# Kernel tuning notes

Measured on AMD Instinct MI355X. Metric: run time of the kernel, lower is better.

Reference implementation:

```python
import jax, jax.numpy as jnp
import numpy as np

EPS = 1e-6
NEG_SLOPE_VEC = 0.2   # VNLeakyReLU default in Pocket2Mol
NEG_SLOPE_SCA = 0.01  # torch nn.LeakyReLU default


def _gvlinear(sca, vec, Wv1, Wv2, Ws, Wg, bg):
    # vec: (n, c_in, 3); Wv1: (c_in, h); Wv2: (h, c_out)
    vh = jnp.einsum('nci,ch->nhi', vec, Wv1)            # VNLinear 1 (no bias)
    vnorm = jnp.sqrt(jnp.sum(vh * vh, axis=-1))          # (n, h)
    out_sca = jnp.concatenate([vnorm, sca], axis=-1) @ Ws  # (n, s_out), no bias
    out_vec = jnp.einsum('nhi,ho->noi', vh, Wv2)         # VNLinear 2 (no bias)
    gate = jax.nn.sigmoid(out_sca @ Wg + bg)[..., None]  # (n, c_out, 1)
    return out_sca, gate * out_vec


def _vn_leaky_relu(vec, Wd):
    # vec: (n, c, 3); Wd: (c, c) learned direction map (no bias)
    d = jnp.einsum('nci,co->noi', vec, Wd)
    dot = jnp.sum(vec * d, axis=-1, keepdims=True)
    d_sq = jnp.sum(d * d, axis=-1, keepdims=True)
    proj = vec - (dot / (d_sq + EPS)) * d
    return NEG_SLOPE_VEC * vec + (1.0 - NEG_SLOPE_VEC) * jnp.where(dot >= 0, vec, proj)


def setup_inputs() -> dict:
    key = jax.random.key(0)
    ks = jax.random.split(key, 13)
    N, M = 400000, 200000
    in_sca, in_vec = 256, 64
    hs, hv = 128, 32
    dh1 = max(in_vec, hv)  # GVLinear layer1 hidden = 64
    dh2 = max(hv, 1)       # GVLinear layer2 hidden = 32

    def w(k, shape, fan_in):
        return jax.random.normal(k, shape, jnp.float32) / np.float32(np.sqrt(fan_in))

    return {
        'h_att_scalar': jax.random.normal(ks[0], (N, in_sca), jnp.float32),
        'h_att_vector': jax.random.normal(ks[1], (N, in_vec, 3), jnp.float32),
        'idx_ligans': jax.random.randint(ks[2], (M,), 0, N),
        # ---- layer 1: GVPerceptronVN (GVLinear + activations) ----
        'Wv1_1': w(ks[3], (in_vec, dh1), in_vec),
        'Wv2_1': w(ks[4], (dh1, hv), dh1),
        'Ws_1':  w(ks[5], (dh1 + in_sca, hs), dh1 + in_sca),
        'Wg_1':  w(ks[6], (hs, hv), hs),
        'bg_1':  jnp.zeros((hv,), jnp.float32),
        'Wd_1':  w(ks[7], (hv, hv), hv),
        # ---- layer 2: GVLinear to (1, 1) ----
        'Wv1_2': w(ks[8], (hv, dh2), hv),
        'Wv2_2': w(ks[9], (dh2, 1), dh2),
        'Ws_2':  w(ks[10], (dh2 + hs, 1), dh2 + hs),
        'Wg_2':  w(ks[11], (1, 1), 1),
        'bg_2':  jnp.zeros((1,), jnp.float32),
    }


def reference(h_att_scalar, h_att_vector, idx_ligans,
              Wv1_1, Wv2_1, Ws_1, Wg_1, bg_1, Wd_1,
              Wv1_2, Wv2_2, Ws_2, Wg_2, bg_2):
    # gather ligand rows
    sca = h_att_scalar[idx_ligans]
    vec = h_att_vector[idx_ligans]
    # GVPerceptronVN
    sca, vec = _gvlinear(sca, vec, Wv1_1, Wv2_1, Ws_1, Wg_1, bg_1)
    vec = _vn_leaky_relu(vec, Wd_1)
    sca = jnp.where(sca >= 0, sca, NEG_SLOPE_SCA * sca)
    # GVLinear -> (1, 1); only scalar branch is returned
    out_sca, _ = _gvlinear(sca, vec, Wv1_2, Wv2_2, Ws_2, Wg_2, bg_2)
    return out_sca  # (M, 1)
```

## Files before the change

### kernel.cpp

```cpp
#include <hip/hip_runtime.h>
#include <math.h>


#define NSV 0.2f
#define NSS 0.01f

__global__ __launch_bounds__(256) void k1_kernel(
    const float* __restrict__ hvec,
    const int*   __restrict__ idx,
    const float* __restrict__ Wv1,
    const float* __restrict__ Wv2,
    float* __restrict__ vnorm_ws,
    float* __restrict__ ovec_ws,
    int M)
{
    __shared__ __align__(16) float sWv1[64*64];
    __shared__ __align__(16) float sWv2[64*32];
    __shared__ __align__(16) float sv[32*196];
    __shared__ int sidx[32];

    const int tid  = threadIdx.x;
    const int row0 = blockIdx.x * 32;

    #pragma unroll
    for (int p = 0; p < 4; ++p) {
        int lin = p*256 + tid;
        *(float4*)&sWv1[lin*4] = *(const float4*)&Wv1[lin*4];
    }
    #pragma unroll
    for (int p = 0; p < 2; ++p) {
        int lin = p*256 + tid;
        *(float4*)&sWv2[lin*4] = *(const float4*)&Wv2[lin*4];
    }
    if (tid < 32) {
        int m = row0 + tid;
        sidx[tid] = idx[m < M ? m : M-1];
    }
    __syncthreads();

    #pragma unroll
    for (int p = 0; p < 6; ++p) {
        int lin = p*256 + tid;
        int r = lin / 48, e4 = lin % 48;
        *(float4*)&sv[r*196 + e4*4] = *(const float4*)&hvec[(size_t)sidx[r]*192 + e4*4];
    }
    __syncthreads();

    const int tx = tid & 15;
    const int ty = tid >> 4;
    float acc[2][4][3];
    #pragma unroll
    for (int a = 0; a < 2; ++a)
        #pragma unroll
        for (int b = 0; b < 4; ++b)
            #pragma unroll
            for (int c = 0; c < 3; ++c) acc[a][b][c] = 0.f;

    for (int c = 0; c < 64; ++c) {
        float av[2][3];
        #pragma unroll
        for (int rr = 0; rr < 2; ++rr) {
            int base = (ty*2 + rr)*196 + c*3;
            av[rr][0] = sv[base+0]; av[rr][1] = sv[base+1]; av[rr][2] = sv[base+2];
        }
        float4 w4 = *(const float4*)&sWv1[c*64 + tx*4];
        float wv[4] = {w4.x, w4.y, w4.z, w4.w};
        #pragma unroll
        for (int rr = 0; rr < 2; ++rr)
            #pragma unroll
            for (int hh = 0; hh < 4; ++hh)
                #pragma unroll
                for (int x = 0; x < 3; ++x)
                    acc[rr][hh][x] += av[rr][x] * wv[hh];
    }

    #pragma unroll
    for (int rr = 0; rr < 2; ++rr) {
        int m = row0 + ty*2 + rr;
        float4 vn;
        vn.x = sqrtf(acc[rr][0][0]*acc[rr][0][0] + acc[rr][0][1]*acc[rr][0][1] + acc[rr][0][2]*acc[rr][0][2]);
        vn.y = sqrtf(acc[rr][1][0]*acc[rr][1][0] + acc[rr][1][1]*acc[rr][1][1] + acc[rr][1][2]*acc[rr][1][2]);
        vn.z = sqrtf(acc[rr][2][0]*acc[rr][2][0] + acc[rr][2][1]*acc[rr][2][1] + acc[rr][2][2]*acc[rr][2][2]);
        vn.w = sqrtf(acc[rr][3][0]*acc[rr][3][0] + acc[rr][3][1]*acc[rr][3][1] + acc[rr][3][2]*acc[rr][3][2]);
        if (m < M) *(float4*)&vnorm_ws[(size_t)m*64 + tx*4] = vn;
    }

    __syncthreads();
    #pragma unroll
    for (int rr = 0; rr < 2; ++rr)
        #pragma unroll
        for (int hh = 0; hh < 4; ++hh)
            #pragma unroll
            for (int x = 0; x < 3; ++x)
                sv[(ty*2 + rr)*196 + (tx*4 + hh)*3 + x] = acc[rr][hh][x];
    __syncthreads();

    const int to = tid & 7;
    const int r2 = tid >> 3;
    float oa[4][3];
    #pragma unroll
    for (int a = 0; a < 4; ++a)
        #pragma unroll
        for (int c = 0; c < 3; ++c) oa[a][c] = 0.f;

    for (int h = 0; h < 64; ++h) {
        int base = r2*196 + h*3;
        float a0 = sv[base+0], a1 = sv[base+1], a2 = sv[base+2];
        float4 w4 = *(const float4*)&sWv2[h*32 + to*4];
        float wv[4] = {w4.x, w4.y, w4.z, w4.w};
        #pragma unroll
        for (int oo = 0; oo < 4; ++oo) {
            oa[oo][0] += a0*wv[oo];
            oa[oo][1] += a1*wv[oo];
            oa[oo][2] += a2*wv[oo];
        }
    }
    int m2 = row0 + r2;
    if (m2 < M) {
        float t[12];
        #pragma unroll
        for (int oo = 0; oo < 4; ++oo)
            #pragma unroll
            for (int x = 0; x < 3; ++x) t[oo*3+x] = oa[oo][x];
        float4* dst = (float4*)&ovec_ws[(size_t)m2*96 + to*12];
        dst[0] = make_float4(t[0], t[1], t[2],  t[3]);
        dst[1] = make_float4(t[4], t[5], t[6],  t[7]);
        dst[2] = make_float4(t[8], t[9], t[10], t[11]);
    }
}

__global__ __launch_bounds__(256) void k2_kernel(
    const float* __restrict__ hsca,
    const int*   __restrict__ idx,
    const float* __restrict__ Ws1,
    const float* __restrict__ vnorm_ws,
    float* __restrict__ osca_ws,
    int M)
{
    __shared__ __align__(16) float sX[128*33];
    __shared__ __align__(16) float sW[32*128];
    __shared__ int sidx[128];

    const int tid  = threadIdx.x;
    const int row0 = blockIdx.x * 128;
    const int tx = tid & 15;
    const int ty = tid >> 4;

    if (tid < 128) {
        int m = row0 + tid;
        sidx[tid] = idx[m < M ? m : M-1];
    }
    __syncthreads();

    const float* xptr[4];
    const float* vptr[4];
    #pragma unroll
    for (int p = 0; p < 4; ++p) {
        int lin = p*256 + tid;
        int r = lin >> 3, c4 = lin & 7;
        int m = row0 + r; if (m >= M) m = M - 1;
        xptr[p] = hsca + (size_t)sidx[r]*256 + c4*4;
        vptr[p] = vnorm_ws + (size_t)m*64 + c4*4;
    }
    const float* wsrc = Ws1 + (size_t)tid*4;

    float4 xr[4], wr[4];

    auto load_tile = [&](int kt) {
        if (kt < 2) {
            #pragma unroll
            for (int p = 0; p < 4; ++p) xr[p] = *(const float4*)(vptr[p] + kt*32);
        } else {
            #pragma unroll
            for (int p = 0; p < 4; ++p) xr[p] = *(const float4*)(xptr[p] + (kt-2)*32);
        }
        const float* w = wsrc + (size_t)kt*4096;
        #pragma unroll
        for (int p = 0; p < 4; ++p) wr[p] = *(const float4*)(w + p*1024);
    };
    auto store_tile = [&]() {
        #pragma unroll
        for (int p = 0; p < 4; ++p) {
            int lin = p*256 + tid;
            int r = lin >> 3, c4 = lin & 7;
            float* d = &sX[r*33 + c4*4];
            d[0] = xr[p].x; d[1] = xr[p].y; d[2] = xr[p].z; d[3] = xr[p].w;
            *(float4*)&sW[lin*4] = wr[p];
        }
    };

    float acc[8][8];
    #pragma unroll
    for (int i = 0; i < 8; ++i)
        #pragma unroll
        for (int j = 0; j < 8; ++j) acc[i][j] = 0.f;

    load_tile(0);
    store_tile();
    load_tile(1);
    __syncthreads();

    #pragma unroll 1
    for (int kt = 0; kt < 10; ++kt) {
        #pragma unroll 8
        for (int k = 0; k < 32; ++k) {
            float a[8];
            #pragma unroll
            for (int rr = 0; rr < 8; ++rr) a[rr] = sX[(ty*8 + rr)*33 + k];
            float4 b0 = *(const float4*)&sW[k*128 + tx*4];
            float4 b1 = *(const float4*)&sW[k*128 + 64 + tx*4];
            float b[8] = {b0.x, b0.y, b0.z, b0.w, b1.x, b1.y, b1.z, b1.w};
            #pragma unroll
            for (int rr = 0; rr < 8; ++rr)
                #pragma unroll
                for (int cc = 0; cc < 8; ++cc)
                    acc[rr][cc] += a[rr] * b[cc];
        }
        if (kt < 9) {
            __syncthreads();
            store_tile();
            if (kt < 8) load_tile(kt + 2);
            __syncthreads();
        }
    }

    #pragma unroll
    for (int rr = 0; rr < 8; ++rr) {
        int m = row0 + ty*8 + rr;
        if (m < M) {
            float4 s0 = make_float4(acc[rr][0], acc[rr][1], acc[rr][2], acc[rr][3]);
            float4 s1 = make_float4(acc[rr][4], acc[rr][5], acc[rr][6], acc[rr][7]);
            *(float4*)&osca_ws[(size_t)m*128 + tx*4]      = s0;
            *(float4*)&osca_ws[(size_t)m*128 + 64 + tx*4] = s1;
        }
    }
}

__global__ __launch_bounds__(256) void k3_kernel(
    const float* __restrict__ osca,
    const float* __restrict__ ovec,
    const float* __restrict__ Wg,
    const float* __restrict__ bg,
    const float* __restrict__ Wd,
    const float* __restrict__ Wv12,
    const float* __restrict__ Ws2,
    float* __restrict__ out,
    int M)
{
    __shared__ __align__(16) float sS[32*132];
    __shared__ __align__(16) float sV[32*100];
    __shared__ __align__(16) float sWg[128*32];
    __shared__ __align__(16) float sWd[32*32];
    __shared__ __align__(16) float sW12[32*32];
    __shared__ float sWs2[160];
    __shared__ float sbg[32];

    const int tid  = threadIdx.x;
    const int row0 = blockIdx.x * 32;

    #pragma unroll
    for (int p = 0; p < 16; ++p) sWg[p*256 + tid] = Wg[p*256 + tid];
    #pragma unroll
    for (int p = 0; p < 4; ++p) {
        sWd[p*256 + tid]  = Wd[p*256 + tid];
        sW12[p*256 + tid] = Wv12[p*256 + tid];
    }
    if (tid < 160) sWs2[tid] = Ws2[tid];
    if (tid < 32)  sbg[tid]  = bg[tid];

    #pragma unroll
    for (int p = 0; p < 16; ++p) {
        int lin = p*256 + tid;
        int r = lin >> 7, j = lin & 127;
        int m = row0 + r; if (m >= M) m = M - 1;
        sS[r*132 + j] = osca[(size_t)m*128 + j];
    }
    #pragma unroll
    for (int p = 0; p < 12; ++p) {
        int lin = p*256 + tid;
        int r = lin / 96, e = lin % 96;
        int m = row0 + r; if (m >= M) m = M - 1;
        sV[r*100 + e] = ovec[(size_t)m*96 + e];
    }
    __syncthreads();

    const int to = tid & 7;
    const int r  = tid >> 3;

    float g[4] = {0.f, 0.f, 0.f, 0.f};
    for (int j = 0; j < 128; ++j) {
        float a = sS[r*132 + j];
        float4 w4 = *(const float4*)&sWg[j*32 + to*4];
        g[0] += a*w4.x; g[1] += a*w4.y; g[2] += a*w4.z; g[3] += a*w4.w;
    }
    float v1[4][3];
    #pragma unroll
    for (int oo = 0; oo < 4; ++oo) {
        int o = to*4 + oo;
        float gt = 1.f / (1.f + __expf(-(g[oo] + sbg[o])));
        #pragma unroll
        for (int x = 0; x < 3; ++x) v1[oo][x] = gt * sV[r*100 + o*3 + x];
    }
    #pragma unroll
    for (int oo = 0; oo < 4; ++oo)
        #pragma unroll
        for (int x = 0; x < 3; ++x)
            sV[r*100 + (to*4 + oo)*3 + x] = v1[oo][x];
    __syncthreads();

    float dd[4][3];
    #pragma unroll
    for (int a = 0; a < 4; ++a)
        #pragma unroll
        for (int c = 0; c < 3; ++c) dd[a][c] = 0.f;
    for (int c = 0; c < 32; ++c) {
        int base = r*100 + c*3;
        float a0 = sV[base+0], a1 = sV[base+1], a2 = sV[base+2];
        float4 w4 = *(const float4*)&sWd[c*32 + to*4];
        float wv[4] = {w4.x, w4.y, w4.z, w4.w};
        #pragma unroll
        for (int oo = 0; oo < 4; ++oo) {
            dd[oo][0] += a0*wv[oo];
            dd[oo][1] += a1*wv[oo];
            dd[oo][2] += a2*wv[oo];
        }
    }
    float v2[4][3];
    #pragma unroll
    for (int oo = 0; oo < 4; ++oo) {
        float dot = v1[oo][0]*dd[oo][0] + v1[oo][1]*dd[oo][1] + v1[oo][2]*dd[oo][2];
        float dsq = dd[oo][0]*dd[oo][0] + dd[oo][1]*dd[oo][1] + dd[oo][2]*dd[oo][2];
        float coef = dot / (dsq + 1e-6f);
        #pragma unroll
        for (int x = 0; x < 3; ++x) {
            float pj = v1[oo][x] - coef*dd[oo][x];
            v2[oo][x] = NSV*v1[oo][x] + (1.f - NSV)*((dot >= 0.f) ? v1[oo][x] : pj);
        }
    }
    __syncthreads();
    #pragma unroll
    for (int oo = 0; oo < 4; ++oo)
        #pragma unroll
        for (int x = 0; x < 3; ++x)
            sV[r*100 + (to*4 + oo)*3 + x] = v2[oo][x];
    __syncthreads();

    float h2[4][3];
    #pragma unroll
    for (int a = 0; a < 4; ++a)
        #pragma unroll
        for (int c = 0; c < 3; ++c) h2[a][c] = 0.f;
    for (int c = 0; c < 32; ++c) {
        int base = r*100 + c*3;
        float a0 = sV[base+0], a1 = sV[base+1], a2 = sV[base+2];
        float4 w4 = *(const float4*)&sW12[c*32 + to*4];
        float wv[4] = {w4.x, w4.y, w4.z, w4.w};
        #pragma unroll
        for (int hh = 0; hh < 4; ++hh) {
            h2[hh][0] += a0*wv[hh];
            h2[hh][1] += a1*wv[hh];
            h2[hh][2] += a2*wv[hh];
        }
    }
    float partial = 0.f;
    #pragma unroll
    for (int hh = 0; hh < 4; ++hh) {
        float vn = sqrtf(h2[hh][0]*h2[hh][0] + h2[hh][1]*h2[hh][1] + h2[hh][2]*h2[hh][2]);
        partial += vn * sWs2[to*4 + hh];
    }
    #pragma unroll
    for (int t = 0; t < 16; ++t) {
        int j = to*16 + t;
        float s = sS[r*132 + j];
        s = (s >= 0.f) ? s : NSS*s;
        partial += s * sWs2[32 + j];
    }
    partial += __shfl_xor(partial, 1);
    partial += __shfl_xor(partial, 2);
    partial += __shfl_xor(partial, 4);
    if (to == 0 && row0 + r < M) out[row0 + r] = partial;
}

extern "C" void kernel_launch(void* const* d_in, const int* in_sizes, int n_in,
                              void* d_out, int out_size, void* d_ws, size_t ws_size,
                              hipStream_t stream) {
    const float* hsca  = (const float*)d_in[0];
    const float* hvec  = (const float*)d_in[1];
    const int*   idx   = (const int*)d_in[2];
    const float* Wv1_1 = (const float*)d_in[3];
    const float* Wv2_1 = (const float*)d_in[4];
    const float* Ws_1  = (const float*)d_in[5];
    const float* Wg_1  = (const float*)d_in[6];
    const float* bg_1  = (const float*)d_in[7];
    const float* Wd_1  = (const float*)d_in[8];
    const float* Wv1_2 = (const float*)d_in[9];
    const float* Ws_2  = (const float*)d_in[11];

    const int M = in_sizes[2];
    float* out = (float*)d_out;

    float* ws       = (float*)d_ws;
    float* vnorm_ws = ws;
    float* ovec_ws  = ws + (size_t)M*64;
    float* osca_ws  = ws + (size_t)M*160;

    const int nb32  = (M + 31) / 32;
    const int nb128 = (M + 127) / 128;

    k1_kernel<<<nb32, 256, 0, stream>>>(hvec, idx, Wv1_1, Wv2_1, vnorm_ws, ovec_ws, M);
    k2_kernel<<<nb128, 256, 0, stream>>>(hsca, idx, Ws_1, vnorm_ws, osca_ws, M);
    k3_kernel<<<nb32, 256, 0, stream>>>(osca_ws, ovec_ws, Wg_1, bg_1, Wd_1, Wv1_2, Ws_2, out, M);
}
```

Before: 1.024 ms.

## Fuse gate and vector tail into scalar GEMM kernel via precomputed Ws1·Wg

```diff
diff --git a/kernel.cpp b/kernel.cpp
--- a/kernel.cpp
+++ b/kernel.cpp
@@ -4,6 +4,19 @@
 
 #define NSV 0.2f
 #define NSS 0.01f
+
+__global__ __launch_bounds__(256) void k0_kernel(
+    const float* __restrict__ Ws1,
+    const float* __restrict__ Wg,
+    float* __restrict__ Wfuse)
+{
+    const int K = blockIdx.x * 8 + (threadIdx.x >> 5);
+    const int o = threadIdx.x & 31;
+    float s = 0.f;
+    for (int j = 0; j < 128; ++j)
+        s += Ws1[K*128 + j] * Wg[j*32 + o];
+    Wfuse[K*32 + o] = s;
+}
 
 __global__ __launch_bounds__(256) void k1_kernel(
     const float* __restrict__ hvec,
@@ -16,8 +29,8 @@
 {
     __shared__ __align__(16) float sWv1[64*64];
     __shared__ __align__(16) float sWv2[64*32];
-    __shared__ __align__(16) float sv[32*196];
-    __shared__ int sidx[32];
+    __shared__ __align__(16) float sv[32*200];
+    __shared__ __align__(16) int sidx[32];
 
     const int tid  = threadIdx.x;
     const int row0 = blockIdx.x * 32;
@@ -42,7 +55,7 @@
     for (int p = 0; p < 6; ++p) {
         int lin = p*256 + tid;
         int r = lin / 48, e4 = lin % 48;
-        *(float4*)&sv[r*196 + e4*4] = *(const float4*)&hvec[(size_t)sidx[r]*192 + e4*4];
+        *(float4*)&sv[r*200 + e4*4] = *(const float4*)&hvec[(size_t)sidx[r]*192 + e4*4];
     }
     __syncthreads();
 
@@ -56,22 +69,27 @@
             #pragma unroll
             for (int c = 0; c < 3; ++c) acc[a][b][c] = 0.f;
 
-    for (int c = 0; c < 64; ++c) {
-        float av[2][3];
+    for (int c = 0; c < 64; c += 4) {
+        float xa[2][12];
         #pragma unroll
         for (int rr = 0; rr < 2; ++rr) {
-            int base = (ty*2 + rr)*196 + c*3;
-            av[rr][0] = sv[base+0]; av[rr][1] = sv[base+1]; av[rr][2] = sv[base+2];
-        }
-        float4 w4 = *(const float4*)&sWv1[c*64 + tx*4];
-        float wv[4] = {w4.x, w4.y, w4.z, w4.w};
-        #pragma unroll
-        for (int rr = 0; rr < 2; ++rr)
-            #pragma unroll
-            for (int hh = 0; hh < 4; ++hh)
+            int base = (ty*2 + rr)*200 + c*3;
+            *(float4*)&xa[rr][0] = *(const float4*)&sv[base];
+            *(float4*)&xa[rr][4] = *(const float4*)&sv[base+4];
+            *(float4*)&xa[rr][8] = *(const float4*)&sv[base+8];
+        }
+        #pragma unroll
+        for (int j = 0; j < 4; ++j) {
+            float4 w4 = *(const float4*)&sWv1[(c+j)*64 + tx*4];
+            float wv[4] = {w4.x, w4.y, w4.z, w4.w};
+            #pragma unroll
+            for (int rr = 0; rr < 2; ++rr)
                 #pragma unroll
-                for (int x = 0; x < 3; ++x)
-                    acc[rr][hh][x] += av[rr][x] * wv[hh];
+                for (int hh = 0; hh < 4; ++hh)
+                    #pragma unroll
+                    for (int x = 0; x < 3; ++x)
+                        acc[rr][hh][x] += xa[rr][j*3 + x] * wv[hh];
+        }
     }
 
     #pragma unroll
@@ -92,7 +110,7 @@
         for (int hh = 0; hh < 4; ++hh)
             #pragma unroll
             for (int x = 0; x < 3; ++x)
-                sv[(ty*2 + rr)*196 + (tx*4 + hh)*3 + x] = acc[rr][hh][x];
+                sv[(ty*2 + rr)*200 + (tx*4 + hh)*3 + x] = acc[rr][hh][x];
     __syncthreads();
 
     const int to = tid & 7;
@@ -103,16 +121,22 @@
         #pragma unroll
         for (int c = 0; c < 3; ++c) oa[a][c] = 0.f;
 
-    for (int h = 0; h < 64; ++h) {
-        int base = r2*196 + h*3;
-        float a0 = sv[base+0], a1 = sv[base+1], a2 = sv[base+2];
-        float4 w4 = *(const float4*)&sWv2[h*32 + to*4];
-        float wv[4] = {w4.x, w4.y, w4.z, w4.w};
-        #pragma unroll
-        for (int oo = 0; oo < 4; ++oo) {
-            oa[oo][0] += a0*wv[oo];
-            oa[oo][1] += a1*wv[oo];
-            oa[oo][2] += a2*wv[oo];
+    for (int h = 0; h < 64; h += 4) {
+        float xa[12];
+        int base = r2*200 + h*3;
+        *(float4*)&xa[0] = *(const float4*)&sv[base];
+        *(float4*)&xa[4] = *(const float4*)&sv[base+4];
+        *(float4*)&xa[8] = *(const float4*)&sv[base+8];
+        #pragma unroll
+        for (int j = 0; j < 4; ++j) {
+            float4 w4 = *(const float4*)&sWv2[(h+j)*32 + to*4];
+            float wv[4] = {w4.x, w4.y, w4.z, w4.w};
+            #pragma unroll
+            for (int oo = 0; oo < 4; ++oo) {
+                oa[oo][0] += xa[j*3+0]*wv[oo];
+                oa[oo][1] += xa[j*3+1]*wv[oo];
+                oa[oo][2] += xa[j*3+2]*wv[oo];
+            }
         }
     }
     int m2 = row0 + r2;
@@ -134,112 +158,8 @@
     const int*   __restrict__ idx,
     const float* __restrict__ Ws1,
     const float* __restrict__ vnorm_ws,
-    float* __restrict__ osca_ws,
-    int M)
-{
-    __shared__ __align__(16) float sX[128*33];
-    __shared__ __align__(16) float sW[32*128];
-    __shared__ int sidx[128];
-
-    const int tid  = threadIdx.x;
-    const int row0 = blockIdx.x * 128;
-    const int tx = tid & 15;
-    const int ty = tid >> 4;
-
-    if (tid < 128) {
-        int m = row0 + tid;
-        sidx[tid] = idx[m < M ? m : M-1];
-    }
-    __syncthreads();
-
-    const float* xptr[4];
-    const float* vptr[4];
-    #pragma unroll
-    for (int p = 0; p < 4; ++p) {
-        int lin = p*256 + tid;
-        int r = lin >> 3, c4 = lin & 7;
-        int m = row0 + r; if (m >= M) m = M - 1;
-        xptr[p] = hsca + (size_t)sidx[r]*256 + c4*4;
-        vptr[p] = vnorm_ws + (size_t)m*64 + c4*4;
-    }
-    const float* wsrc = Ws1 + (size_t)tid*4;
-
-    float4 xr[4], wr[4];
-
-    auto load_tile = [&](int kt) {
-        if (kt < 2) {
-            #pragma unroll
-            for (int p = 0; p < 4; ++p) xr[p] = *(const float4*)(vptr[p] + kt*32);
-        } else {
-            #pragma unroll
-            for (int p = 0; p < 4; ++p) xr[p] = *(const float4*)(xptr[p] + (kt-2)*32);
-        }
-        const float* w = wsrc + (size_t)kt*4096;
-        #pragma unroll
-        for (int p = 0; p < 4; ++p) wr[p] = *(const float4*)(w + p*1024);
-    };
-    auto store_tile = [&]() {
-        #pragma unroll
-        for (int p = 0; p < 4; ++p) {
-            int lin = p*256 + tid;
-            int r = lin >> 3, c4 = lin & 7;
-            float* d = &sX[r*33 + c4*4];
-            d[0] = xr[p].x; d[1] = xr[p].y; d[2] = xr[p].z; d[3] = xr[p].w;
-            *(float4*)&sW[lin*4] = wr[p];
-        }
-    };
-
-    float acc[8][8];
-    #pragma unroll
-    for (int i = 0; i < 8; ++i)
-        #pragma unroll
-        for (int j = 0; j < 8; ++j) acc[i][j] = 0.f;
-
-    load_tile(0);
-    store_tile();
-    load_tile(1);
-    __syncthreads();
-
-    #pragma unroll 1
-    for (int kt = 0; kt < 10; ++kt) {
-        #pragma unroll 8
-        for (int k = 0; k < 32; ++k) {
-            float a[8];
-            #pragma unroll
-            for (int rr = 0; rr < 8; ++rr) a[rr] = sX[(ty*8 + rr)*33 + k];
-            float4 b0 = *(const float4*)&sW[k*128 + tx*4];
-            float4 b1 = *(const float4*)&sW[k*128 + 64 + tx*4];
-            float b[8] = {b0.x, b0.y, b0.z, b0.w, b1.x, b1.y, b1.z, b1.w};
-            #pragma unroll
-            for (int rr = 0; rr < 8; ++rr)
-                #pragma unroll
-                for (int cc = 0; cc < 8; ++cc)
-                    acc[rr][cc] += a[rr] * b[cc];
-        }
-        if (kt < 9) {
-            __syncthreads();
-            store_tile();
-            if (kt < 8) load_tile(kt + 2);
-            __syncthreads();
-        }
-    }
-
-    #pragma unroll
-    for (int rr = 0; rr < 8; ++rr) {
-        int m = row0 + ty*8 + rr;
-        if (m < M) {
-            float4 s0 = make_float4(acc[rr][0], acc[rr][1], acc[rr][2], acc[rr][3]);
-            float4 s1 = make_float4(acc[rr][4], acc[rr][5], acc[rr][6], acc[rr][7]);
-            *(float4*)&osca_ws[(size_t)m*128 + tx*4]      = s0;
-            *(float4*)&osca_ws[(size_t)m*128 + 64 + tx*4] = s1;
-        }
-    }
-}
-
-__global__ __launch_bounds__(256) void k3_kernel(
-    const float* __restrict__ osca,
-    const float* __restrict__ ovec,
-    const float* __restrict__ Wg,
+    const float* __restrict__ ovec_ws,
+    const float* __restrict__ Wfuse,
     const float* __restrict__ bg,
     const float* __restrict__ Wd,
     const float* __restrict__ Wv12,
@@ -247,138 +167,237 @@
     float* __restrict__ out,
     int M)
 {
-    __shared__ __align__(16) float sS[32*132];
-    __shared__ __align__(16) float sV[32*100];
-    __shared__ __align__(16) float sWg[128*32];
+    __shared__ __align__(16) float sXT[32*132];
+    __shared__ __align__(16) float sW[32*128];
+    __shared__ __align__(16) float sG[32*32];
+    __shared__ __align__(16) float sV[64*101];
     __shared__ __align__(16) float sWd[32*32];
     __shared__ __align__(16) float sW12[32*32];
-    __shared__ float sWs2[160];
-    __shared__ float sbg[32];
+    __shared__ __align__(16) float sWs2[160];
+    __shared__ __align__(16) float sSca[128];
+    __shared__ __align__(16) int   sidx[128];
 
     const int tid  = threadIdx.x;
-    const int row0 = blockIdx.x * 32;
-
-    #pragma unroll
-    for (int p = 0; p < 16; ++p) sWg[p*256 + tid] = Wg[p*256 + tid];
+    const int row0 = blockIdx.x * 128;
+    const int tx = tid & 15;
+    const int ty = tid >> 4;
+
+    if (tid < 128) {
+        int m = row0 + tid;
+        sidx[tid] = idx[m < M ? m : M-1];
+    }
+    {
+        int lin = tid;
+        *(float4*)&sWd[lin*4]  = *(const float4*)&Wd[lin*4];
+        *(float4*)&sW12[lin*4] = *(const float4*)&Wv12[lin*4];
+        if (tid < 160) sWs2[tid] = Ws2[tid];
+    }
+    __syncthreads();
+
+    const float* xptr[4];
+    const float* vptr[4];
     #pragma unroll
     for (int p = 0; p < 4; ++p) {
-        sWd[p*256 + tid]  = Wd[p*256 + tid];
-        sW12[p*256 + tid] = Wv12[p*256 + tid];
-    }
-    if (tid < 160) sWs2[tid] = Ws2[tid];
-    if (tid < 32)  sbg[tid]  = bg[tid];
-
-    #pragma unroll
-    for (int p = 0; p < 16; ++p) {
         int lin = p*256 + tid;
-        int r = lin >> 7, j = lin & 127;
+        int r = lin >> 3, c4 = lin & 7;
         int m = row0 + r; if (m >= M) m = M - 1;
-        sS[r*132 + j] = osca[(size_t)m*128 + j];
-    }
-    #pragma unroll
-    for (int p = 0; p < 12; ++p) {
-        int lin = p*256 + tid;
-        int r = lin / 96, e = lin % 96;
-        int m = row0 + r; if (m >= M) m = M - 1;
-        sV[r*100 + e] = ovec[(size_t)m*96 + e];
-    }
-    __syncthreads();
-
-    const int to = tid & 7;
-    const int r  = tid >> 3;
-
-    float g[4] = {0.f, 0.f, 0.f, 0.f};
-    for (int j = 0; j < 128; ++j) {
-        float a = sS[r*132 + j];
-        float4 w4 = *(const float4*)&sWg[j*32 + to*4];
-        g[0] += a*w4.x; g[1] += a*w4.y; g[2] += a*w4.z; g[3] += a*w4.w;
-    }
-    float v1[4][3];
-    #pragma unroll
-    for (int oo = 0; oo < 4; ++oo) {
-        int o = to*4 + oo;
-        float gt = 1.f / (1.f + __expf(-(g[oo] + sbg[o])));
-        #pragma unroll
-        for (int x = 0; x < 3; ++x) v1[oo][x] = gt * sV[r*100 + o*3 + x];
-    }
-    #pragma unroll
-    for (int oo = 0; oo < 4; ++oo)
-        #pragma unroll
-        for (int x = 0; x < 3; ++x)
-            sV[r*100 + (to*4 + oo)*3 + x] = v1[oo][x];
-    __syncthreads();
-
-    float dd[4][3];
-    #pragma unroll
-    for (int a = 0; a < 4; ++a)
-        #pragma unroll
-        for (int c = 0; c < 3; ++c) dd[a][c] = 0.f;
-    for (int c = 0; c < 32; ++c) {
-        int base = r*100 + c*3;
-        float a0 = sV[base+0], a1 = sV[base+1], a2 = sV[base+2];
-        float4 w4 = *(const float4*)&sWd[c*32 + to*4];
-        float wv[4] = {w4.x, w4.y, w4.z, w4.w};
-        #pragma unroll
-        for (int oo = 0; oo < 4; ++oo) {
-            dd[oo][0] += a0*wv[oo];
-            dd[oo][1] += a1*wv[oo];
-            dd[oo][2] += a2*wv[oo];
-        }
-    }
-    float v2[4][3];
-    #pragma unroll
-    for (int oo = 0; oo < 4; ++oo) {
-        float dot = v1[oo][0]*dd[oo][0] + v1[oo][1]*dd[oo][1] + v1[oo][2]*dd[oo][2];
-        float dsq = dd[oo][0]*dd[oo][0] + dd[oo][1]*dd[oo][1] + dd[oo][2]*dd[oo][2];
-        float coef = dot / (dsq + 1e-6f);
-        #pragma unroll
-        for (int x = 0; x < 3; ++x) {
-            float pj = v1[oo][x] - coef*dd[oo][x];
-            v2[oo][x] = NSV*v1[oo][x] + (1.f - NSV)*((dot >= 0.f) ? v1[oo][x] : pj);
-        }
-    }
-    __syncthreads();
-    #pragma unroll
-    for (int oo = 0; oo < 4; ++oo)
-        #pragma unroll
-        for (int x = 0; x < 3; ++x)
-            sV[r*100 + (to*4 + oo)*3 + x] = v2[oo][x];
-    __syncthreads();
-
-    float h2[4][3];
-    #pragma unroll
-    for (int a = 0; a < 4; ++a)
-        #pragma unroll
-        for (int c = 0; c < 3; ++c) h2[a][c] = 0.f;
-    for (int c = 0; c < 32; ++c) {
-        int base = r*100 + c*3;
-        float a0 = sV[base+0], a1 = sV[base+1], a2 = sV[base+2];
-        float4 w4 = *(const float4*)&sW12[c*32 + to*4];
-        float wv[4] = {w4.x, w4.y, w4.z, w4.w};
-        #pragma unroll
-        for (int hh = 0; hh < 4; ++hh) {
-            h2[hh][0] += a0*wv[hh];
-            h2[hh][1] += a1*wv[hh];
-            h2[hh][2] += a2*wv[hh];
-        }
-    }
-    float partial = 0.f;
-    #pragma unroll
-    for (int hh = 0; hh < 4; ++hh) {
-        float vn = sqrtf(h2[hh][0]*h2[hh][0] + h2[hh][1]*h2[hh][1] + h2[hh][2]*h2[hh][2]);
-        partial += vn * sWs2[to*4 + hh];
-    }
-    #pragma unroll
-    for (int t = 0; t < 16; ++t) {
-        int j = to*16 + t;
-        float s = sS[r*132 + j];
-        s = (s >= 0.f) ? s : NSS*s;
-        partial += s * sWs2[32 + j];
-    }
-    partial += __shfl_xor(partial, 1);
-    partial += __shfl_xor(partial, 2);
-    partial += __shfl_xor(partial, 4);
-    if (to == 0 && row0 + r < M) out[row0 + r] = partial;
+        xptr[p] = hsca + (size_t)sidx[r]*256 + c4*4;
+        vptr[p] = vnorm_ws + (size_t)m*64 + c4*4;
+    }
+    const float* wsrc = Ws1 + (size_t)tid*4;
+    const float* gsrc = Wfuse + (size_t)tid*4;
+
+    float4 xr[4], wr[4], gr;
+
+    auto load_tile = [&](int kt) {
+        if (kt < 2) {
+            #pragma unroll
+            for (int p = 0; p < 4; ++p) xr[p] = *(const float4*)(vptr[p] + kt*32);
+        } else {
+            #pragma unroll
+            for (int p = 0; p < 4; ++p) xr[p] = *(const float4*)(xptr[p] + (kt-2)*32);
+        }
+        const float* w = wsrc + (size_t)kt*4096;
+        #pragma unroll
+        for (int p = 0; p < 4; ++p) wr[p] = *(const float4*)(w + p*1024);
+        gr = *(const float4*)(gsrc + (size_t)kt*1024);
+    };
+    auto store_tile = [&]() {
+        #pragma unroll
+        for (int p = 0; p < 4; ++p) {
+            int lin = p*256 + tid;
+            int r = lin >> 3, c4 = lin & 7;
+            int kb = c4*4;
+            sXT[(kb+0)*132 + r] = xr[p].x;
+            sXT[(kb+1)*132 + r] = xr[p].y;
+            sXT[(kb+2)*132 + r] = xr[p].z;
+            sXT[(kb+3)*132 + r] = xr[p].w;
+            *(float4*)&sW[lin*4] = wr[p];
+        }
+        *(float4*)&sG[tid*4] = gr;
+    };
+
+    float acc[8][8];
+    float accg[8][2];
+    #pragma unroll
+    for (int i = 0; i < 8; ++i) {
+        #pragma unroll
+        for (int j = 0; j < 8; ++j) acc[i][j] = 0.f;
+        accg[i][0] = 0.f; accg[i][1] = 0.f;
+    }
+
+    load_tile(0);
+    store_tile();
+    load_tile(1);
+    __syncthreads();
+
+    #pragma unroll 1
+    for (int kt = 0; kt < 10; ++kt) {
+        #pragma unroll 8
+        for (int k = 0; k < 32; ++k) {
+            float4 A0 = *(const float4*)&sXT[k*132 + ty*8];
+            float4 A1 = *(const float4*)&sXT[k*132 + ty*8 + 4];
+            float4 b0 = *(const float4*)&sW[k*128 + tx*4];
+            float4 b1 = *(const float4*)&sW[k*128 + 64 + tx*4];
+            float2 gg = *(const float2*)&sG[k*32 + tx*2];
+            float a[8] = {A0.x, A0.y, A0.z, A0.w, A1.x, A1.y, A1.z, A1.w};
+            float b[8] = {b0.x, b0.y, b0.z, b0.w, b1.x, b1.y, b1.z, b1.w};
+            #pragma unroll
+            for (int rr = 0; rr < 8; ++rr) {
+                #pragma unroll
+                for (int cc = 0; cc < 8; ++cc)
+                    acc[rr][cc] += a[rr] * b[cc];
+                accg[rr][0] += a[rr] * gg.x;
+                accg[rr][1] += a[rr] * gg.y;
+            }
+        }
+        if (kt < 9) {
+            __syncthreads();
+            store_tile();
+            if (kt < 8) load_tile(kt + 2);
+            __syncthreads();
+        }
+    }
+
+    {
+        float4 wA = *(const float4*)&sWs2[32 + tx*4];
+        float4 wB = *(const float4*)&sWs2[32 + 64 + tx*4];
+        float wv[8] = {wA.x, wA.y, wA.z, wA.w, wB.x, wB.y, wB.z, wB.w};
+        #pragma unroll
+        for (int rr = 0; rr < 8; ++rr) {
+            float p = 0.f;
+            #pragma unroll
+            for (int cc = 0; cc < 8; ++cc) {
+                float s = acc[rr][cc];
+                float l = (s >= 0.f) ? s : NSS*s;
+                p += l * wv[cc];
+            }
+            p += __shfl_xor(p, 1);
+            p += __shfl_xor(p, 2);
+            p += __shfl_xor(p, 4);
+            p += __shfl_xor(p, 8);
+            if (tx == 0) sSca[ty*8 + rr] = p;
+        }
+    }
+
+    const float bg0 = bg[tx*2], bg1 = bg[tx*2 + 1];
+    const int lr2 = tid >> 2, q = tid & 3;
+
+    #pragma unroll 1
+    for (int ch = 0; ch < 2; ++ch) {
+        __syncthreads();
+
+        if ((ty >> 3) == ch) {
+            int tyl = ty & 7;
+            #pragma unroll
+            for (int rr = 0; rr < 8; ++rr) {
+                int lr = tyl*8 + rr;
+                int m = row0 + ch*64 + lr; if (m >= M) m = M - 1;
+                const float* op = ovec_ws + (size_t)m*96 + tx*6;
+                float g0 = 1.f / (1.f + __expf(-(accg[rr][0] + bg0)));
+                float g1 = 1.f / (1.f + __expf(-(accg[rr][1] + bg1)));
+                float* vd = &sV[lr*101 + tx*6];
+                vd[0] = g0*op[0]; vd[1] = g0*op[1]; vd[2] = g0*op[2];
+                vd[3] = g1*op[3]; vd[4] = g1*op[4]; vd[5] = g1*op[5];
+            }
+        }
+        __syncthreads();
+
+        float dd[8][3];
+        #pragma unroll
+        for (int a = 0; a < 8; ++a)
+            #pragma unroll
+            for (int x = 0; x < 3; ++x) dd[a][x] = 0.f;
+        for (int c = 0; c < 32; ++c) {
+            float vx = sV[lr2*101 + c*3 + 0];
+            float vy = sV[lr2*101 + c*3 + 1];
+            float vz = sV[lr2*101 + c*3 + 2];
+            float4 w0 = *(const float4*)&sWd[c*32 + q*8];
+            float4 w1 = *(const float4*)&sWd[c*32 + q*8 + 4];
+            float wv[8] = {w0.x, w0.y, w0.z, w0.w, w1.x, w1.y, w1.z, w1.w};
+            #pragma unroll
+            for (int oo = 0; oo < 8; ++oo) {
+                dd[oo][0] += vx*wv[oo];
+                dd[oo][1] += vy*wv[oo];
+                dd[oo][2] += vz*wv[oo];
+            }
+        }
+        float v2[8][3];
+        #pragma unroll
+        for (int oo = 0; oo < 8; ++oo) {
+            int o = q*8 + oo;
+            float v1x = sV[lr2*101 + o*3 + 0];
+            float v1y = sV[lr2*101 + o*3 + 1];
+            float v1z = sV[lr2*101 + o*3 + 2];
+            float dot = v1x*dd[oo][0] + v1y*dd[oo][1] + v1z*dd[oo][2];
+            float dsq = dd[oo][0]*dd[oo][0] + dd[oo][1]*dd[oo][1] + dd[oo][2]*dd[oo][2];
+            float coef = dot / (dsq + 1e-6f);
+            float px = v1x - coef*dd[oo][0];
+            float py = v1y - coef*dd[oo][1];
+            float pz = v1z - coef*dd[oo][2];
+            v2[oo][0] = NSV*v1x + (1.f - NSV)*((dot >= 0.f) ? v1x : px);
+            v2[oo][1] = NSV*v1y + (1.f - NSV)*((dot >= 0.f) ? v1y : py);
+            v2[oo][2] = NSV*v1z + (1.f - NSV)*((dot >= 0.f) ? v1z : pz);
+        }
+        __syncthreads();
+        #pragma unroll
+        for (int oo = 0; oo < 8; ++oo) {
+            sV[lr2*101 + (q*8+oo)*3 + 0] = v2[oo][0];
+            sV[lr2*101 + (q*8+oo)*3 + 1] = v2[oo][1];
+            sV[lr2*101 + (q*8+oo)*3 + 2] = v2[oo][2];
+        }
+        __syncthreads();
+
+        float h2[8][3];
+        #pragma unroll
+        for (int a = 0; a < 8; ++a)
+            #pragma unroll
+            for (int x = 0; x < 3; ++x) h2[a][x] = 0.f;
+        for (int c = 0; c < 32; ++c) {
+            float vx = sV[lr2*101 + c*3 + 0];
+            float vy = sV[lr2*101 + c*3 + 1];
+            float vz = sV[lr2*101 + c*3 + 2];
+            float4 w0 = *(const float4*)&sW12[c*32 + q*8];
+            float4 w1 = *(const float4*)&sW12[c*32 + q*8 + 4];
+            float wv[8] = {w0.x, w0.y, w0.z, w0.w, w1.x, w1.y, w1.z, w1.w};
+            #pragma unroll
+            for (int hh = 0; hh < 8; ++hh) {
+                h2[hh][0] += vx*wv[hh];
+                h2[hh][1] += vy*wv[hh];
+                h2[hh][2] += vz*wv[hh];
+            }
+        }
+        float partial = 0.f;
+        #pragma unroll
+        for (int hh = 0; hh < 8; ++hh) {
+            float vn = sqrtf(h2[hh][0]*h2[hh][0] + h2[hh][1]*h2[hh][1] + h2[hh][2]*h2[hh][2]);
+            partial += vn * sWs2[q*8 + hh];
+        }
+        partial += __shfl_xor(partial, 1);
+        partial += __shfl_xor(partial, 2);
+        int m = row0 + ch*64 + lr2;
+        if (q == 0 && m < M) out[m] = partial + sSca[ch*64 + lr2];
+    }
 }
 
 extern "C" void kernel_launch(void* const* d_in, const int* in_sizes, int n_in,
@@ -402,12 +421,13 @@
     float* ws       = (float*)d_ws;
     float* vnorm_ws = ws;
     float* ovec_ws  = ws + (size_t)M*64;
-    float* osca_ws  = ws + (size_t)M*160;
+    float* wfuse_ws = ws + (size_t)M*160;
 
     const int nb32  = (M + 31) / 32;
     const int nb128 = (M + 127) / 128;
 
+    k0_kernel<<<40, 256, 0, stream>>>(Ws_1, Wg_1, wfuse_ws);
     k1_kernel<<<nb32, 256, 0, stream>>>(hvec, idx, Wv1_1, Wv2_1, vnorm_ws, ovec_ws, M);
-    k2_kernel<<<nb128, 256, 0, stream>>>(hsca, idx, Ws_1, vnorm_ws, osca_ws, M);
-    k3_kernel<<<nb32, 256, 0, stream>>>(osca_ws, ovec_ws, Wg_1, bg_1, Wd_1, Wv1_2, Ws_2, out, M);
+    k2_kernel<<<nb128, 256, 0, stream>>>(hsca, idx, Ws_1, vnorm_ws, ovec_ws, wfuse_ws,
+                                         bg_1, Wd_1, Wv1_2, Ws_2, out, M);
 }
```

Measured after the change: 1.214 ms. 18.6% more time.
